# Kernel optimization log

Measured on AMD Instinct MI355X. Metric: run time of the kernel, lower is better.

Reference implementation:

```python
import jax, jax.numpy as jnp
import numpy as np

N = 100000   # nodes
E = 1600000  # edges (before self loops)
H = 2        # attention heads
C = 32       # per-head channels
EPS_BN = 1e-5
NEG_SLOPE = 0.2


def setup_inputs():
    key = jax.random.key(0)
    ks = jax.random.split(key, 32)
    s = 0.1
    inp = {
        "h": jax.random.normal(ks[0], (N, 2), jnp.float32),
        "edge_index": jax.random.randint(ks[1], (2, E), 0, N, dtype=jnp.int32),
        "bn_gamma": jnp.ones((2,), jnp.float32),
        "bn_beta": jnp.zeros((2,), jnp.float32),
        # GATConv 1: in=2 -> H*C=64
        "W1": jax.random.normal(ks[2], (H * C, 2), jnp.float32) * s,
        "as1": jax.random.normal(ks[3], (H, C), jnp.float32) * s,
        "ad1": jax.random.normal(ks[4], (H, C), jnp.float32) * s,
        "b1": jnp.zeros((H * C,), jnp.float32),
        # GATConv 2: in=64 -> 64
        "W2": jax.random.normal(ks[5], (H * C, 64), jnp.float32) * s,
        "as2": jax.random.normal(ks[6], (H, C), jnp.float32) * s,
        "ad2": jax.random.normal(ks[7], (H, C), jnp.float32) * s,
        "b2": jnp.zeros((H * C,), jnp.float32),
    }
    dims = [(64, 64), (64, 64), (64, 64), (64, 64), (11, 64)]
    for i, (o, ii) in enumerate(dims, start=1):
        inp[f"fw{i}"] = jax.random.normal(ks[8 + 2 * i], (o, ii), jnp.float32) * s
        inp[f"fb{i}"] = jnp.zeros((o,), jnp.float32)
    return inp


def _gat_layer(x, src, dst, W, a_src, a_dst, b):
    # x: [N, Fin] -> xp: [N, H, C]
    xp = (x @ W.T).reshape(N, H, C)
    e_src = jnp.einsum("nhc,hc->nh", xp, a_src)  # [N,H]
    e_dst = jnp.einsum("nhc,hc->nh", xp, a_dst)
    e = jax.nn.leaky_relu(e_src[src] + e_dst[dst], NEG_SLOPE)  # [Etot,H]
    # segment softmax over incoming edges of each dst node
    m = jax.ops.segment_max(e, dst, num_segments=N)            # [N,H]
    ex = jnp.exp(e - m[dst])
    denom = jax.ops.segment_sum(ex, dst, num_segments=N)
    alpha = ex / (denom[dst] + 1e-16)                          # [Etot,H]
    out = jax.ops.segment_sum(xp[src] * alpha[:, :, None], dst, num_segments=N)
    return out.reshape(N, H * C) + b


def reference(h, edge_index, bn_gamma, bn_beta,
              W1, as1, ad1, b1, W2, as2, ad2, b2,
              fw1, fb1, fw2, fb2, fw3, fb3, fw4, fb4, fw5, fb5):
    # BatchNorm1d (training mode: batch statistics, biased variance)
    mu = h.mean(0)
    var = ((h - mu) ** 2).mean(0)
    x = (h - mu) * jax.lax.rsqrt(var + EPS_BN) * bn_gamma + bn_beta

    # add self loops (PyG GATConv default)
    ar = jnp.arange(N, dtype=edge_index.dtype)
    src = jnp.concatenate([edge_index[0], ar])
    dst = jnp.concatenate([edge_index[1], ar])

    x = jax.nn.relu(_gat_layer(x, src, dst, W1, as1, ad1, b1))
    x = jax.nn.relu(_gat_layer(x, src, dst, W2, as2, ad2, b2))

    x = jax.nn.relu(x @ fw1.T + fb1)
    x = jax.nn.relu(x @ fw2.T + fb2)
    x = jax.nn.relu(x @ fw3.T + fb3)
    x = jax.nn.relu(x @ fw4.T + fb4)
    return x @ fw5.T + fb5
```

## Files before the change

### kernel.cpp

```cpp
#include <hip/hip_runtime.h>
#include <hip/hip_fp16.h>
#include <math.h>

#define NN 100000
#define EE 1600000
#define ET (EE + NN)
#define NEG 0.2f
#define SMASK 0x1FFFF

#define NBUCK 196
#define NBLK 416
#define BITEMS 4096
#define BCAP 10240

typedef float4 f4;
typedef _Float16 h8 __attribute__((ext_vector_type(8)));
typedef float f32x4 __attribute__((ext_vector_type(4)));

__global__ void k_init(float* stats, int* gcnt,
                       const float* __restrict__ W1, const float* __restrict__ as1,
                       const float* __restrict__ ad1, float* __restrict__ coef) {
    int i = threadIdx.x;
    if (i < 4) stats[i] = 0.f;
    if (i < NBUCK) gcnt[i] = 0;
    if (i >= 248) {
        int t = i - 248;
        int sd = t >> 2, hh = (t >> 1) & 1, c0 = t & 1;
        const float* a = sd ? ad1 : as1;
        float s = 0.f;
        for (int c = 0; c < 32; ++c) s += W1[(hh * 32 + c) * 2 + c0] * a[hh * 32 + c];
        coef[t] = s;
    }
}

__global__ void k_bnstats(const float* __restrict__ h, float* stats) {
    __shared__ float red[16];
    int gid = blockIdx.x * blockDim.x + threadIdx.x;
    int stride = gridDim.x * blockDim.x;
    float s0 = 0.f, s1 = 0.f, q0 = 0.f, q1 = 0.f;
    for (int i = gid; i < NN; i += stride) {
        float2 v = reinterpret_cast<const float2*>(h)[i];
        s0 += v.x; q0 += v.x * v.x;
        s1 += v.y; q1 += v.y * v.y;
    }
#pragma unroll
    for (int off = 32; off >= 1; off >>= 1) {
        s0 += __shfl_xor(s0, off);
        s1 += __shfl_xor(s1, off);
        q0 += __shfl_xor(q0, off);
        q1 += __shfl_xor(q1, off);
    }
    int wv = threadIdx.x >> 6;
    if ((threadIdx.x & 63) == 0) {
        red[wv * 4 + 0] = s0; red[wv * 4 + 1] = s1;
        red[wv * 4 + 2] = q0; red[wv * 4 + 3] = q1;
    }
    __syncthreads();
    if (threadIdx.x == 0) {
        float t0 = 0.f, t1 = 0.f, t2 = 0.f, t3 = 0.f;
#pragma unroll
        for (int i = 0; i < 4; ++i) {
            t0 += red[i * 4 + 0]; t1 += red[i * 4 + 1];
            t2 += red[i * 4 + 2]; t3 += red[i * 4 + 3];
        }
        atomicAdd(&stats[0], t0); atomicAdd(&stats[1], t1);
        atomicAdd(&stats[2], t2); atomicAdd(&stats[3], t3);
    }
}

__global__ void k_wprep(const float* __restrict__ W2g,
                        const float* __restrict__ w1, const float* __restrict__ w2,
                        const float* __restrict__ w3, const float* __restrict__ w4,
                        const float* __restrict__ w5,
                        _Float16* __restrict__ BH, _Float16* __restrict__ BL,
                        _Float16* __restrict__ BH5, _Float16* __restrict__ BL5) {
    int idx = blockIdx.x * blockDim.x + threadIdx.x;
    if (idx < 5 * 4096) {
        int L = idx >> 12;
        int r = idx & 4095;
        int ks = r >> 11, nt = (r >> 9) & 3, lane = (r >> 3) & 63, j = r & 7;
        const float* W = (L == 0) ? w1 : (L == 1) ? w2 : (L == 2) ? w3 : (L == 3) ? w4 : W2g;
        int n = nt * 16 + (lane & 15);
        int k = ks * 32 + 8 * (lane >> 4) + j;
        float v = W[n * 64 + k];
        _Float16 hi = (_Float16)v;
        BH[idx] = hi;
        BL[idx] = (_Float16)(v - (float)hi);
    }
    if (idx < 1024) {
        int ks = idx >> 9, lane = (idx >> 3) & 63, j = idx & 7;
        int n = lane & 15;
        int k = ks * 32 + 8 * (lane >> 4) + j;
        float v = (n < 11) ? w5[n * 64 + k] : 0.f;
        _Float16 hi = (_Float16)v;
        BH5[idx] = hi;
        BL5[idx] = (_Float16)(v - (float)hi);
    }
}

__global__ void __launch_bounds__(256) k_fpart(const int* __restrict__ ei, int* gcnt,
                                               unsigned* __restrict__ pairs) {
    __shared__ int hist[NBUCK];
    __shared__ int cur[NBUCK];
    int tid = threadIdx.x, blk = blockIdx.x;
    if (tid < NBUCK) hist[tid] = 0;
    int ss[16], dd[16];
    int base = blk * BITEMS;
    __syncthreads();
#pragma unroll
    for (int it = 0; it < 16; ++it) {
        int i = base + it * 256 + tid;
        int s = 0, d = -1;
        if (i < ET) {
            if (i < EE) { s = ei[i]; d = ei[EE + i]; }
            else { s = d = i - EE; }
            atomicAdd(&hist[d >> 9], 1);
        }
        ss[it] = s; dd[it] = d;
    }
    __syncthreads();
    if (tid < NBUCK) cur[tid] = tid * BCAP + atomicAdd(&gcnt[tid], hist[tid]);
    __syncthreads();
#pragma unroll
    for (int it = 0; it < 16; ++it) {
        int d = dd[it];
        if (d >= 0) {
            int pos = atomicAdd(&cur[d >> 9], 1);
            pairs[pos] = (unsigned)ss[it] | ((unsigned)(d & 511) << 17);
        }
    }
}

__global__ void __launch_bounds__(512) k_bucket(const unsigned* __restrict__ pairs,
                                                 const int* __restrict__ gcnt,
                                                 int* __restrict__ rowptr,
                                                 unsigned* __restrict__ srcl) {
    __shared__ int sh[512];
    __shared__ int se[512];
    int b = blockIdx.x, tid = threadIdx.x;
    sh[tid] = (tid < b) ? gcnt[tid] : 0;
    __syncthreads();
    for (int off = 256; off >= 1; off >>= 1) {
        if (tid < off) sh[tid] += sh[tid + off];
        __syncthreads();
    }
    int obase = sh[0];
    __syncthreads();
    int cnt = gcnt[b];
    int ibase = b * BCAP;
    sh[tid] = 0;
    __syncthreads();
    for (int k = tid; k < cnt; k += 512) atomicAdd(&sh[pairs[ibase + k] >> 17], 1);
    __syncthreads();
    int deg = sh[tid];
    se[tid] = deg;
    __syncthreads();
    for (int off = 1; off < 512; off <<= 1) {
        int t = (tid >= off) ? se[tid - off] : 0;
        __syncthreads();
        se[tid] += t;
        __syncthreads();
    }
    int excl = se[tid] - deg;
    int node = (b << 9) + tid;
    if (node < NN) rowptr[node] = obase + excl;
    sh[tid] = obase + excl;
    __syncthreads();
    for (int k = tid; k < cnt; k += 512) {
        unsigned p = pairs[ibase + k];
        int pos = atomicAdd(&sh[p >> 17], 1);
        srcl[pos] = p;
    }
    if (b == 0 && tid == 0) rowptr[NN] = ET;
}

__global__ void k_prep1(const float* __restrict__ h, const float* __restrict__ stats,
                        const float* __restrict__ gamma, const float* __restrict__ beta,
                        const float* __restrict__ coef,
                        f4* __restrict__ nd1, float2* __restrict__ ed1) {
    int n = blockIdx.x * blockDim.x + threadIdx.x;
    if (n >= NN) return;
    const float inv = 1.f / (float)NN;
    float mu0 = stats[0] * inv, mu1 = stats[1] * inv;
    float v0 = stats[2] * inv - mu0 * mu0;
    float v1 = stats[3] * inv - mu1 * mu1;
    float g0 = rsqrtf(v0 + 1e-5f) * gamma[0];
    float g1 = rsqrtf(v1 + 1e-5f) * gamma[1];
    float2 hv = reinterpret_cast<const float2*>(h)[n];
    float x0 = (hv.x - mu0) * g0 + beta[0];
    float x1 = (hv.y - mu1) * g1 + beta[1];
    nd1[n] = make_float4(x0 * coef[0] + x1 * coef[1], x0 * coef[2] + x1 * coef[3], x0, x1);
    ed1[n] = make_float2(x0 * coef[4] + x1 * coef[5], x0 * coef[6] + x1 * coef[7]);
}

__global__ void __launch_bounds__(256) k_gat1(
    const f4* __restrict__ nd1, const float2* __restrict__ ed1,
    const int* __restrict__ rowptr, const unsigned* __restrict__ srcl,
    f4* __restrict__ agg1a, float2* __restrict__ agg1s) {
    int gid = blockIdx.x * blockDim.x + threadIdx.x;
    int n = gid >> 3;
    int sub = gid & 7;
    if (n >= NN) return;
    int beg = rowptr[n], end = rowptr[n + 1];
    float2 ed = ed1[n];
    float A0 = 0.f, B0 = 0.f, S0 = 0.f, A1 = 0.f, B1 = 0.f, S1 = 0.f;
    for (int k = beg + sub; k < end; k += 8) {
        int s = (int)(srcl[k] & SMASK);
        f4 p = nd1[s];
        float e0 = p.x + ed.x;
        float e1 = p.y + ed.y;
        e0 = fmaxf(e0, NEG * e0);
        e1 = fmaxf(e1, NEG * e1);
        float w0 = __expf(e0);
        float w1 = __expf(e1);
        A0 += w0 * p.z; B0 += w0 * p.w; S0 += w0;
        A1 += w1 * p.z; B1 += w1 * p.w; S1 += w1;
    }
#pragma unroll
    for (int off = 1; off < 8; off <<= 1) {
        A0 += __shfl_xor(A0, off);
        B0 += __shfl_xor(B0, off);
        S0 += __shfl_xor(S0, off);
        A1 += __shfl_xor(A1, off);
        B1 += __shfl_xor(B1, off);
        S1 += __shfl_xor(S1, off);
    }
    if (sub == 0) {
        agg1a[n] = make_float4(A0, B0, A1, B1);
        agg1s[n] = make_float2(S0, S1);
    }
}

#define MAKE_A(ks)                                                                \
    f4 a0 = *reinterpret_cast<const f4*>(&xw[mrow * 68 + kg * 8 + (ks) * 32]);    \
    f4 a1 = *reinterpret_cast<const f4*>(&xw[mrow * 68 + kg * 8 + (ks) * 32 + 4]);\
    float av0 = a0.x, av1 = a0.y, av2 = a0.z, av3 = a0.w;                         \
    float av4 = a1.x, av5 = a1.y, av6 = a1.z, av7 = a1.w;                         \
    h8 ah, al;                                                                    \
    { _Float16 t;                                                                 \
      t = (_Float16)av0; ah[0] = t; al[0] = (_Float16)(av0 - (float)t);           \
      t = (_Float16)av1; ah[1] = t; al[1] = (_Float16)(av1 - (float)t);           \
      t = (_Float16)av2; ah[2] = t; al[2] = (_Float16)(av2 - (float)t);           \
      t = (_Float16)av3; ah[3] = t; al[3] = (_Float16)(av3 - (float)t);           \
      t = (_Float16)av4; ah[4] = t; al[4] = (_Float16)(av4 - (float)t);           \
      t = (_Float16)av5; ah[5] = t; al[5] = (_Float16)(av5 - (float)t);           \
      t = (_Float16)av6; ah[6] = t; al[6] = (_Float16)(av6 - (float)t);           \
      t = (_Float16)av7; ah[7] = t; al[7] = (_Float16)(av7 - (float)t); }

__global__ void __launch_bounds__(256) k_xform2m(
    const f4* __restrict__ agg1a, const float2* __restrict__ agg1s,
    const float* __restrict__ W1, const float* __restrict__ b1,
    const _Float16* __restrict__ BH2, const _Float16* __restrict__ BL2,
    const float* __restrict__ a_s, const float* __restrict__ a_d,
    __half* __restrict__ xph, float2* __restrict__ es2v, float2* __restrict__ ed2v) {
    __shared__ float xs[4 * 1088];
    int lane = threadIdx.x & 63;
    int w = threadIdx.x >> 6;
    float* xw = &xs[w * 1088];
    int nodeBase = blockIdx.x * 64 + w * 16;
    int mrow = lane & 15;
    int kg = lane >> 4;
    int n = nodeBase + mrow;

    f4 ag = make_float4(0.f, 0.f, 0.f, 0.f);
    float2 sg = make_float2(1.f, 1.f);
    if (n < NN) { ag = agg1a[n]; sg = agg1s[n]; }
    float r0 = 1.f / (sg.x + 1e-16f);
    float r1 = 1.f / (sg.y + 1e-16f);
#pragma unroll
    for (int j = 0; j < 16; ++j) {
        int f = kg * 16 + j;
        float A = (f < 32) ? ag.x : ag.z;
        float B = (f < 32) ? ag.y : ag.w;
        float r = (f < 32) ? r0 : r1;
        xw[mrow * 68 + f] = fmaxf((A * W1[2 * f] + B * W1[2 * f + 1]) * r + b1[f], 0.f);
    }
    __syncthreads();

    const h8* bh = reinterpret_cast<const h8*>(BH2);
    const h8* bl = reinterpret_cast<const h8*>(BL2);
    h8 BHr[2][4], BLr[2][4];
#pragma unroll
    for (int ks = 0; ks < 2; ++ks)
#pragma unroll
        for (int nt = 0; nt < 4; ++nt) {
            BHr[ks][nt] = bh[(ks * 4 + nt) * 64 + lane];
            BLr[ks][nt] = bl[(ks * 4 + nt) * 64 + lane];
        }
    f32x4 acc0 = {0.f, 0.f, 0.f, 0.f}, acc1 = acc0, acc2 = acc0, acc3 = acc0;
#pragma unroll
    for (int ks = 0; ks < 2; ++ks) {
        MAKE_A(ks)
        acc0 = __builtin_amdgcn_mfma_f32_16x16x32_f16(ah, BHr[ks][0], acc0, 0, 0, 0);
        acc1 = __builtin_amdgcn_mfma_f32_16x16x32_f16(ah, BHr[ks][1], acc1, 0, 0, 0);
        acc2 = __builtin_amdgcn_mfma_f32_16x16x32_f16(ah, BHr[ks][2], acc2, 0, 0, 0);
        acc3 = __builtin_amdgcn_mfma_f32_16x16x32_f16(ah, BHr[ks][3], acc3, 0, 0, 0);
        acc0 = __builtin_amdgcn_mfma_f32_16x16x32_f16(ah, BLr[ks][0], acc0, 0, 0, 0);
        acc1 = __builtin_amdgcn_mfma_f32_16x16x32_f16(ah, BLr[ks][1], acc1, 0, 0, 0);
        acc2 = __builtin_amdgcn_mfma_f32_16x16x32_f16(ah, BLr[ks][2], acc2, 0, 0, 0);
        acc3 = __builtin_amdgcn_mfma_f32_16x16x32_f16(ah, BLr[ks][3], acc3, 0, 0, 0);
        acc0 = __builtin_amdgcn_mfma_f32_16x16x32_f16(al, BHr[ks][0], acc0, 0, 0, 0);
        acc1 = __builtin_amdgcn_mfma_f32_16x16x32_f16(al, BHr[ks][1], acc1, 0, 0, 0);
        acc2 = __builtin_amdgcn_mfma_f32_16x16x32_f16(al, BHr[ks][2], acc2, 0, 0, 0);
        acc3 = __builtin_amdgcn_mfma_f32_16x16x32_f16(al, BHr[ks][3], acc3, 0, 0, 0);
    }
    __syncthreads();
#pragma unroll
    for (int r = 0; r < 4; ++r) {
        int row = 4 * kg + r;
        xw[row * 68 + mrow]      = acc0[r];
        xw[row * 68 + 16 + mrow] = acc1[r];
        xw[row * 68 + 32 + mrow] = acc2[r];
        xw[row * 68 + 48 + mrow] = acc3[r];
    }
    __syncthreads();

    float ps = 0.f, pd = 0.f;
#pragma unroll
    for (int j = 0; j < 16; ++j) {
        int f = kg * 16 + j;
        float v = xw[mrow * 68 + f];
        ps += v * a_s[f];
        pd += v * a_d[f];
    }
    ps += __shfl_xor(ps, 16);
    pd += __shfl_xor(pd, 16);
    float psB = __shfl_xor(ps, 32);
    float pdB = __shfl_xor(pd, 32);
    if (kg == 0 && n < NN) {
        es2v[n] = make_float2(ps, psB);
        ed2v[n] = make_float2(pd, pdB);
    }

#pragma unroll
    for (int i = 0; i < 8; ++i) {
        int idx = lane + 64 * i;
        int nl = idx >> 5;
        int c = idx & 31;
        int g = nodeBase + nl;
        if (g < NN) {
            __half2 hv = __floats2half2_rn(xw[nl * 68 + 2 * c], xw[nl * 68 + 2 * c + 1]);
            *reinterpret_cast<__half2*>(&xph[(size_t)g * 64 + 2 * c]) = hv;
        }
    }
}

__global__ void __launch_bounds__(256) k_gat2(
    const __half* __restrict__ xph, const float2* __restrict__ es2v,
    const float2* __restrict__ ed2v,
    const int* __restrict__ rowptr, const unsigned* __restrict__ srcl,
    const float* __restrict__ bias, float* __restrict__ y) {
    int wid = (blockIdx.x * blockDim.x + threadIdx.x) >> 6;
    int lane = threadIdx.x & 63;
    if (wid >= NN) return;
    int g = lane >> 3;
    int t = lane & 7;
    bool hh = t >= 4;
    int ch = 8 * t;
    float2 edp = ed2v[wid];
    float edv = hh ? edp.y : edp.x;
    int beg = rowptr[wid], end = rowptr[wid + 1];
    float sum = 0.f;
    float a0 = 0.f, a1 = 0.f, a2 = 0.f, a3 = 0.f;
    float a4 = 0.f, a5 = 0.f, a6 = 0.f, a7 = 0.f;
    int k = beg;

#define GO(kk)                                                                    \
    {                                                                             \
        int s_ = (int)(srcl[(kk) + g] & SMASK);                                   \
        float2 ep_ = es2v[s_];                                                    \
        uint4 xr_ = *reinterpret_cast<const uint4*>(&xph[(size_t)s_ * 64 + ch]);  \
        float e_ = (hh ? ep_.y : ep_.x) + edv;                                    \
        e_ = fmaxf(e_, NEG * e_);                                                 \
        float w_ = __expf(e_);                                                    \
        float2 p0_ = __half22float2(*reinterpret_cast<const __half2*>(&xr_.x));   \
        float2 p1_ = __half22float2(*reinterpret_cast<const __half2*>(&xr_.y));   \
        float2 p2_ = __half22float2(*reinterpret_cast<const __half2*>(&xr_.z));   \
        float2 p3_ = __half22float2(*reinterpret_cast<const __half2*>(&xr_.w));   \
        sum += w_;                                                                \
        a0 += w_ * p0_.x; a1 += w_ * p0_.y; a2 += w_ * p1_.x; a3 += w_ * p1_.y;   \
        a4 += w_ * p2_.x; a5 += w_ * p2_.y; a6 += w_ * p3_.x; a7 += w_ * p3_.y;   \
    }

    for (; k + 16 <= end; k += 16) {
        GO(k) GO(k + 8)
    }
    for (; k + 8 <= end; k += 8) {
        GO(k)
    }
    if (k < end) {
        int idx = k + g;
        bool valid = idx < end;
        int s_ = (int)(srcl[valid ? idx : k] & SMASK);
        float2 ep_ = es2v[s_];
        uint4 xr_ = *reinterpret_cast<const uint4*>(&xph[(size_t)s_ * 64 + ch]);
        float e_ = (hh ? ep_.y : ep_.x) + edv;
        e_ = fmaxf(e_, NEG * e_);
        float w_ = valid ? __expf(e_) : 0.f;
        float2 p0_ = __half22float2(*reinterpret_cast<const __half2*>(&xr_.x));
        float2 p1_ = __half22float2(*reinterpret_cast<const __half2*>(&xr_.y));
        float2 p2_ = __half22float2(*reinterpret_cast<const __half2*>(&xr_.z));
        float2 p3_ = __half22float2(*reinterpret_cast<const __half2*>(&xr_.w));
        sum += w_;
        a0 += w_ * p0_.x; a1 += w_ * p0_.y; a2 += w_ * p1_.x; a3 += w_ * p1_.y;
        a4 += w_ * p2_.x; a5 += w_ * p2_.y; a6 += w_ * p3_.x; a7 += w_ * p3_.y;
    }
#undef GO

#pragma unroll
    for (int off = 8; off <= 32; off <<= 1) {
        sum += __shfl_xor(sum, off);
        a0 += __shfl_xor(a0, off); a1 += __shfl_xor(a1, off);
        a2 += __shfl_xor(a2, off); a3 += __shfl_xor(a3, off);
        a4 += __shfl_xor(a4, off); a5 += __shfl_xor(a5, off);
        a6 += __shfl_xor(a6, off); a7 += __shfl_xor(a7, off);
    }
    if (lane < 8) {
        float rs = 1.f / (sum + 1e-16f);
        f4 r0v, r1v;
        r0v.x = fmaxf(a0 * rs + bias[ch], 0.f);
        r0v.y = fmaxf(a1 * rs + bias[ch + 1], 0.f);
        r0v.z = fmaxf(a2 * rs + bias[ch + 2], 0.f);
        r0v.w = fmaxf(a3 * rs + bias[ch + 3], 0.f);
        r1v.x = fmaxf(a4 * rs + bias[ch + 4], 0.f);
        r1v.y = fmaxf(a5 * rs + bias[ch + 5], 0.f);
        r1v.z = fmaxf(a6 * rs + bias[ch + 6], 0.f);
        r1v.w = fmaxf(a7 * rs + bias[ch + 7], 0.f);
        *reinterpret_cast<f4*>(&y[(size_t)wid * 64 + ch]) = r0v;
        *reinterpret_cast<f4*>(&y[(size_t)wid * 64 + ch + 4]) = r1v;
    }
}

__global__ void __launch_bounds__(256) k_mlp(
    const float* __restrict__ hin,
    const _Float16* __restrict__ BH, const _Float16* __restrict__ BL,
    const _Float16* __restrict__ BH5, const _Float16* __restrict__ BL5,
    const float* __restrict__ b1, const float* __restrict__ b2,
    const float* __restrict__ b3, const float* __restrict__ b4,
    const float* __restrict__ b5,
    float* __restrict__ out) {
    __shared__ float xs[4 * 16 * 68];
    int lane = threadIdx.x & 63;
    int w = threadIdx.x >> 6;
    float* xw = &xs[w * 1088];
    int nodeBase = blockIdx.x * 64 + w * 16;
    int mrow = lane & 15;
    int kg = lane >> 4;

#pragma unroll
    for (int i = 0; i < 4; ++i) {
        int v = lane + 64 * i;
        int nl = v >> 4;
        int c4 = v & 15;
        f4 t = make_float4(0.f, 0.f, 0.f, 0.f);
        if (nodeBase + nl < NN)
            t = reinterpret_cast<const f4*>(hin)[(size_t)(nodeBase + nl) * 16 + c4];
        *reinterpret_cast<f4*>(&xw[nl * 68 + c4 * 4]) = t;
    }
    __syncthreads();

#define MLP_LAYER(L, Bp)                                                          \
    {                                                                             \
        const h8* bh = reinterpret_cast<const h8*>(BH + (L) * 4096);              \
        const h8* bl = reinterpret_cast<const h8*>(BL + (L) * 4096);              \
        h8 BHr[2][4], BLr[2][4];                                                  \
        _Pragma("unroll")                                                         \
        for (int ks = 0; ks < 2; ++ks)                                            \
            _Pragma("unroll")                                                     \
            for (int nt = 0; nt < 4; ++nt) {                                      \
                BHr[ks][nt] = bh[(ks * 4 + nt) * 64 + lane];                      \
                BLr[ks][nt] = bl[(ks * 4 + nt) * 64 + lane];                      \
            }                                                                     \
        float bj0 = Bp[mrow], bj1 = Bp[16 + mrow];                                \
        float bj2 = Bp[32 + mrow], bj3 = Bp[48 + mrow];                           \
        f32x4 acc0 = {0.f, 0.f, 0.f, 0.f}, acc1 = acc0, acc2 = acc0, acc3 = acc0; \
        _Pragma("unroll")                                                         \
        for (int ks = 0; ks < 2; ++ks) {                                          \
            MAKE_A(ks)                                                            \
            acc0 = __builtin_amdgcn_mfma_f32_16x16x32_f16(ah, BHr[ks][0], acc0, 0, 0, 0); \
            acc1 = __builtin_amdgcn_mfma_f32_16x16x32_f16(ah, BHr[ks][1], acc1, 0, 0, 0); \
            acc2 = __builtin_amdgcn_mfma_f32_16x16x32_f16(ah, BHr[ks][2], acc2, 0, 0, 0); \
            acc3 = __builtin_amdgcn_mfma_f32_16x16x32_f16(ah, BHr[ks][3], acc3, 0, 0, 0); \
            acc0 = __builtin_amdgcn_mfma_f32_16x16x32_f16(ah, BLr[ks][0], acc0, 0, 0, 0); \
            acc1 = __builtin_amdgcn_mfma_f32_16x16x32_f16(ah, BLr[ks][1], acc1, 0, 0, 0); \
            acc2 = __builtin_amdgcn_mfma_f32_16x16x32_f16(ah, BLr[ks][2], acc2, 0, 0, 0); \
            acc3 = __builtin_amdgcn_mfma_f32_16x16x32_f16(ah, BLr[ks][3], acc3, 0, 0, 0); \
            acc0 = __builtin_amdgcn_mfma_f32_16x16x32_f16(al, BHr[ks][0], acc0, 0, 0, 0); \
            acc1 = __builtin_amdgcn_mfma_f32_16x16x32_f16(al, BHr[ks][1], acc1, 0, 0, 0); \
            acc2 = __builtin_amdgcn_mfma_f32_16x16x32_f16(al, BHr[ks][2], acc2, 0, 0, 0); \
            acc3 = __builtin_amdgcn_mfma_f32_16x16x32_f16(al, BHr[ks][3], acc3, 0, 0, 0); \
        }                                                                         \
        __syncthreads();                                                          \
        _Pragma("unroll")                                                         \
        for (int r = 0; r < 4; ++r) {                                             \
            int row = 4 * kg + r;                                                 \
            xw[row * 68 + mrow]      = fmaxf(acc0[r] + bj0, 0.f);                 \
            xw[row * 68 + 16 + mrow] = fmaxf(acc1[r] + bj1, 0.f);                 \
            xw[row * 68 + 32 + mrow] = fmaxf(acc2[r] + bj2, 0.f);                 \
            xw[row * 68 + 48 + mrow] = fmaxf(acc3[r] + bj3, 0.f);                 \
        }                                                                         \
        __syncthreads();                                                          \
    }

    MLP_LAYER(0, b1)
    MLP_LAYER(1, b2)
    MLP_LAYER(2, b3)
    MLP_LAYER(3, b4)
#undef MLP_LAYER

    {
        const h8* bh = reinterpret_cast<const h8*>(BH5);
        const h8* bl = reinterpret_cast<const h8*>(BL5);
        f32x4 acc = {0.f, 0.f, 0.f, 0.f};
#pragma unroll
        for (int ks = 0; ks < 2; ++ks) {
            MAKE_A(ks)
            h8 b_h = bh[ks * 64 + lane];
            h8 b_l = bl[ks * 64 + lane];
            acc = __builtin_amdgcn_mfma_f32_16x16x32_f16(ah, b_h, acc, 0, 0, 0);
            acc = __builtin_amdgcn_mfma_f32_16x16x32_f16(ah, b_l, acc, 0, 0, 0);
            acc = __builtin_amdgcn_mfma_f32_16x16x32_f16(al, b_h, acc, 0, 0, 0);
        }
        if (mrow < 11) {
            float b5v = b5[mrow];
#pragma unroll
            for (int r = 0; r < 4; ++r) {
                int node = nodeBase + 4 * kg + r;
                if (node < NN) out[(size_t)node * 11 + mrow] = acc[r] + b5v;
            }
        }
    }
}

extern "C" void kernel_launch(void* const* d_in, const int* in_sizes, int n_in,
                              void* d_out, int out_size, void* d_ws, size_t ws_size,
                              hipStream_t stream) {
    const float* h   = (const float*)d_in[0];
    const int*   ei  = (const int*)d_in[1];
    const float* gam = (const float*)d_in[2];
    const float* bet = (const float*)d_in[3];
    const float* W1  = (const float*)d_in[4];
    const float* as1 = (const float*)d_in[5];
    const float* ad1 = (const float*)d_in[6];
    const float* b1  = (const float*)d_in[7];
    const float* W2  = (const float*)d_in[8];
    const float* as2 = (const float*)d_in[9];
    const float* ad2 = (const float*)d_in[10];
    const float* b2  = (const float*)d_in[11];
    const float* fw1 = (const float*)d_in[12];
    const float* fb1 = (const float*)d_in[13];
    const float* fw2 = (const float*)d_in[14];
    const float* fb2 = (const float*)d_in[15];
    const float* fw3 = (const float*)d_in[16];
    const float* fb3 = (const float*)d_in[17];
    const float* fw4 = (const float*)d_in[18];
    const float* fb4 = (const float*)d_in[19];
    const float* fw5 = (const float*)d_in[20];
    const float* fb5 = (const float*)d_in[21];
    float* out = (float*)d_out;

    char* ws = (char*)d_ws;
    size_t off = 0;
    auto alloc = [&](size_t bytes) -> char* {
        char* p = ws + off;
        off += (bytes + 255) & ~(size_t)255;
        return p;
    };
    float* stats  = (float*)alloc(4 * sizeof(float));
    float* coef   = (float*)alloc(8 * sizeof(float));
    int*   gcnt   = (int*)alloc(NBUCK * sizeof(int));
    int*   rowptr = (int*)alloc((size_t)(NN + 1) * sizeof(int));
    unsigned* srcl = (unsigned*)alloc((size_t)ET * sizeof(unsigned));
    float2* es2v  = (float2*)alloc((size_t)NN * sizeof(float2));
    float2* ed2v  = (float2*)alloc((size_t)NN * sizeof(float2));
    _Float16* BH  = (_Float16*)alloc(5 * 4096 * sizeof(_Float16));
    _Float16* BL  = (_Float16*)alloc(5 * 4096 * sizeof(_Float16));
    _Float16* BH5 = (_Float16*)alloc(1024 * sizeof(_Float16));
    _Float16* BL5 = (_Float16*)alloc(1024 * sizeof(_Float16));
    float* bufA   = (float*)alloc((size_t)NN * 64 * sizeof(float));
    float* bufB   = (float*)alloc((size_t)NN * 64 * sizeof(float));
    unsigned* pairs = (unsigned*)bufA;
    __half* xph   = (__half*)bufA;
    f4*     agg1a = (f4*)bufB;
    float2* agg1s = (float2*)(bufB + 400000);
    f4*     nd1   = (f4*)(bufB + 600000);
    float2* ed1   = (float2*)(bufB + 1000000);
    (void)ws_size; (void)in_sizes; (void)n_in; (void)out_size;

    k_init<<<1, 256, 0, stream>>>(stats, gcnt, W1, as1, ad1, coef);
    k_bnstats<<<64, 256, 0, stream>>>(h, stats);
    k_wprep<<<96, 256, 0, stream>>>(W2, fw1, fw2, fw3, fw4, fw5, BH, BL, BH5, BL5);

    k_fpart<<<NBLK, 256, 0, stream>>>(ei, gcnt, pairs);
    k_bucket<<<NBUCK, 512, 0, stream>>>(pairs, gcnt, rowptr, srcl);

    k_prep1<<<(NN + 255) / 256, 256, 0, stream>>>(h, stats, gam, bet, coef, nd1, ed1);
    k_gat1<<<(NN * 8 + 255) / 256, 256, 0, stream>>>(nd1, ed1, rowptr, srcl, agg1a, agg1s);

    k_xform2m<<<(NN + 63) / 64, 256, 0, stream>>>(agg1a, agg1s, W1, b1,
                                                  BH + 4 * 4096, BL + 4 * 4096,
                                                  as2, ad2, xph, es2v, ed2v);

    k_gat2<<<(NN * 64) / 256, 256, 0, stream>>>(xph, es2v, ed2v, rowptr, srcl, b2, bufB);

    k_mlp<<<(NN + 63) / 64, 256, 0, stream>>>(bufB, BH, BL, BH5, BL5,
                                              fb1, fb2, fb3, fb4, fb5, out);
}
```

Baseline: 151.7 us.

## Merge setup kernels, fuse BN prep into bucket, store GAT2 output as fp16

Merges the init and weight-prep kernels into a single launch and folds the per-node BatchNorm/attention-coefficient prep into the bucket-sort kernel, cutting two kernel launches. It also makes the second GAT layer write its activations as fp16 and has the MLP read and widen them, halving that intermediate's traffic. The fp16 intermediate adds rounding error to the MLP input.

```diff
diff --git a/kernel.cpp b/kernel.cpp
--- a/kernel.cpp
+++ b/kernel.cpp
@@ -17,64 +17,29 @@
 typedef _Float16 h8 __attribute__((ext_vector_type(8)));
 typedef float f32x4 __attribute__((ext_vector_type(4)));
 
-__global__ void k_init(float* stats, int* gcnt,
-                       const float* __restrict__ W1, const float* __restrict__ as1,
-                       const float* __restrict__ ad1, float* __restrict__ coef) {
-    int i = threadIdx.x;
-    if (i < 4) stats[i] = 0.f;
-    if (i < NBUCK) gcnt[i] = 0;
-    if (i >= 248) {
-        int t = i - 248;
-        int sd = t >> 2, hh = (t >> 1) & 1, c0 = t & 1;
-        const float* a = sd ? ad1 : as1;
-        float s = 0.f;
-        for (int c = 0; c < 32; ++c) s += W1[(hh * 32 + c) * 2 + c0] * a[hh * 32 + c];
-        coef[t] = s;
-    }
-}
-
-__global__ void k_bnstats(const float* __restrict__ h, float* stats) {
-    __shared__ float red[16];
-    int gid = blockIdx.x * blockDim.x + threadIdx.x;
-    int stride = gridDim.x * blockDim.x;
-    float s0 = 0.f, s1 = 0.f, q0 = 0.f, q1 = 0.f;
-    for (int i = gid; i < NN; i += stride) {
-        float2 v = reinterpret_cast<const float2*>(h)[i];
-        s0 += v.x; q0 += v.x * v.x;
-        s1 += v.y; q1 += v.y * v.y;
-    }
-#pragma unroll
-    for (int off = 32; off >= 1; off >>= 1) {
-        s0 += __shfl_xor(s0, off);
-        s1 += __shfl_xor(s1, off);
-        q0 += __shfl_xor(q0, off);
-        q1 += __shfl_xor(q1, off);
-    }
-    int wv = threadIdx.x >> 6;
-    if ((threadIdx.x & 63) == 0) {
-        red[wv * 4 + 0] = s0; red[wv * 4 + 1] = s1;
-        red[wv * 4 + 2] = q0; red[wv * 4 + 3] = q1;
-    }
-    __syncthreads();
-    if (threadIdx.x == 0) {
-        float t0 = 0.f, t1 = 0.f, t2 = 0.f, t3 = 0.f;
-#pragma unroll
-        for (int i = 0; i < 4; ++i) {
-            t0 += red[i * 4 + 0]; t1 += red[i * 4 + 1];
-            t2 += red[i * 4 + 2]; t3 += red[i * 4 + 3];
-        }
-        atomicAdd(&stats[0], t0); atomicAdd(&stats[1], t1);
-        atomicAdd(&stats[2], t2); atomicAdd(&stats[3], t3);
-    }
-}
-
-__global__ void k_wprep(const float* __restrict__ W2g,
+__global__ void k_setup(float* stats, int* gcnt,
+                        const float* __restrict__ W1, const float* __restrict__ as1,
+                        const float* __restrict__ ad1, float* __restrict__ coef,
+                        const float* __restrict__ W2g,
                         const float* __restrict__ w1, const float* __restrict__ w2,
                         const float* __restrict__ w3, const float* __restrict__ w4,
                         const float* __restrict__ w5,
                         _Float16* __restrict__ BH, _Float16* __restrict__ BL,
                         _Float16* __restrict__ BH5, _Float16* __restrict__ BL5) {
     int idx = blockIdx.x * blockDim.x + threadIdx.x;
+    if (blockIdx.x == 0) {
+        int i = threadIdx.x;
+        if (i < 4) stats[i] = 0.f;
+        if (i < NBUCK) gcnt[i] = 0;
+        if (i >= 248) {
+            int t = i - 248;
+            int sd = t >> 2, hh = (t >> 1) & 1, c0 = t & 1;
+            const float* a = sd ? ad1 : as1;
+            float s = 0.f;
+            for (int c = 0; c < 32; ++c) s += W1[(hh * 32 + c) * 2 + c0] * a[hh * 32 + c];
+            coef[t] = s;
+        }
+    }
     if (idx < 5 * 4096) {
         int L = idx >> 12;
         int r = idx & 4095;
@@ -98,6 +63,41 @@
     }
 }
 
+__global__ void k_bnstats(const float* __restrict__ h, float* stats) {
+    __shared__ float red[16];
+    int gid = blockIdx.x * blockDim.x + threadIdx.x;
+    int stride = gridDim.x * blockDim.x;
+    float s0 = 0.f, s1 = 0.f, q0 = 0.f, q1 = 0.f;
+    for (int i = gid; i < NN; i += stride) {
+        float2 v = reinterpret_cast<const float2*>(h)[i];
+        s0 += v.x; q0 += v.x * v.x;
+        s1 += v.y; q1 += v.y * v.y;
+    }
+#pragma unroll
+    for (int off = 32; off >= 1; off >>= 1) {
+        s0 += __shfl_xor(s0, off);
+        s1 += __shfl_xor(s1, off);
+        q0 += __shfl_xor(q0, off);
+        q1 += __shfl_xor(q1, off);
+    }
+    int wv = threadIdx.x >> 6;
+    if ((threadIdx.x & 63) == 0) {
+        red[wv * 4 + 0] = s0; red[wv * 4 + 1] = s1;
+        red[wv * 4 + 2] = q0; red[wv * 4 + 3] = q1;
+    }
+    __syncthreads();
+    if (threadIdx.x == 0) {
+        float t0 = 0.f, t1 = 0.f, t2 = 0.f, t3 = 0.f;
+#pragma unroll
+        for (int i = 0; i < 4; ++i) {
+            t0 += red[i * 4 + 0]; t1 += red[i * 4 + 1];
+            t2 += red[i * 4 + 2]; t3 += red[i * 4 + 3];
+        }
+        atomicAdd(&stats[0], t0); atomicAdd(&stats[1], t1);
+        atomicAdd(&stats[2], t2); atomicAdd(&stats[3], t3);
+    }
+}
+
 __global__ void __launch_bounds__(256) k_fpart(const int* __restrict__ ei, int* gcnt,
                                                unsigned* __restrict__ pairs) {
     __shared__ int hist[NBUCK];
@@ -134,7 +134,13 @@
 __global__ void __launch_bounds__(512) k_bucket(const unsigned* __restrict__ pairs,
                                                  const int* __restrict__ gcnt,
                                                  int* __restrict__ rowptr,
-                                                 unsigned* __restrict__ srcl) {
+                                                 unsigned* __restrict__ srcl,
+                                                 const float* __restrict__ h,
+                                                 const float* __restrict__ stats,
+                                                 const float* __restrict__ gamma,
+                                                 const float* __restrict__ beta,
+                                                 const float* __restrict__ coef,
+                                                 f4* __restrict__ nd1, float2* __restrict__ ed1) {
     __shared__ int sh[512];
     __shared__ int se[512];
     int b = blockIdx.x, tid = threadIdx.x;
@@ -172,25 +178,20 @@
         srcl[pos] = p;
     }
     if (b == 0 && tid == 0) rowptr[NN] = ET;
-}
-
-__global__ void k_prep1(const float* __restrict__ h, const float* __restrict__ stats,
-                        const float* __restrict__ gamma, const float* __restrict__ beta,
-                        const float* __restrict__ coef,
-                        f4* __restrict__ nd1, float2* __restrict__ ed1) {
-    int n = blockIdx.x * blockDim.x + threadIdx.x;
-    if (n >= NN) return;
-    const float inv = 1.f / (float)NN;
-    float mu0 = stats[0] * inv, mu1 = stats[1] * inv;
-    float v0 = stats[2] * inv - mu0 * mu0;
-    float v1 = stats[3] * inv - mu1 * mu1;
-    float g0 = rsqrtf(v0 + 1e-5f) * gamma[0];
-    float g1 = rsqrtf(v1 + 1e-5f) * gamma[1];
-    float2 hv = reinterpret_cast<const float2*>(h)[n];
-    float x0 = (hv.x - mu0) * g0 + beta[0];
-    float x1 = (hv.y - mu1) * g1 + beta[1];
-    nd1[n] = make_float4(x0 * coef[0] + x1 * coef[1], x0 * coef[2] + x1 * coef[3], x0, x1);
-    ed1[n] = make_float2(x0 * coef[4] + x1 * coef[5], x0 * coef[6] + x1 * coef[7]);
+
+    if (node < NN) {
+        const float inv = 1.f / (float)NN;
+        float mu0 = stats[0] * inv, mu1 = stats[1] * inv;
+        float v0 = stats[2] * inv - mu0 * mu0;
+        float v1 = stats[3] * inv - mu1 * mu1;
+        float g0 = rsqrtf(v0 + 1e-5f) * gamma[0];
+        float g1 = rsqrtf(v1 + 1e-5f) * gamma[1];
+        float2 hv = reinterpret_cast<const float2*>(h)[node];
+        float x0 = (hv.x - mu0) * g0 + beta[0];
+        float x1 = (hv.y - mu1) * g1 + beta[1];
+        nd1[node] = make_float4(x0 * coef[0] + x1 * coef[1], x0 * coef[2] + x1 * coef[3], x0, x1);
+        ed1[node] = make_float2(x0 * coef[4] + x1 * coef[5], x0 * coef[6] + x1 * coef[7]);
+    }
 }
 
 __global__ void __launch_bounds__(256) k_gat1(
@@ -349,7 +350,7 @@
     const __half* __restrict__ xph, const float2* __restrict__ es2v,
     const float2* __restrict__ ed2v,
     const int* __restrict__ rowptr, const unsigned* __restrict__ srcl,
-    const float* __restrict__ bias, float* __restrict__ y) {
+    const float* __restrict__ bias, __half* __restrict__ yh) {
     int wid = (blockIdx.x * blockDim.x + threadIdx.x) >> 6;
     int lane = threadIdx.x & 63;
     if (wid >= NN) return;
@@ -417,22 +418,25 @@
     }
     if (lane < 8) {
         float rs = 1.f / (sum + 1e-16f);
-        f4 r0v, r1v;
-        r0v.x = fmaxf(a0 * rs + bias[ch], 0.f);
-        r0v.y = fmaxf(a1 * rs + bias[ch + 1], 0.f);
-        r0v.z = fmaxf(a2 * rs + bias[ch + 2], 0.f);
-        r0v.w = fmaxf(a3 * rs + bias[ch + 3], 0.f);
-        r1v.x = fmaxf(a4 * rs + bias[ch + 4], 0.f);
-        r1v.y = fmaxf(a5 * rs + bias[ch + 5], 0.f);
-        r1v.z = fmaxf(a6 * rs + bias[ch + 6], 0.f);
-        r1v.w = fmaxf(a7 * rs + bias[ch + 7], 0.f);
-        *reinterpret_cast<f4*>(&y[(size_t)wid * 64 + ch]) = r0v;
-        *reinterpret_cast<f4*>(&y[(size_t)wid * 64 + ch + 4]) = r1v;
+        __half2 o0 = __floats2half2_rn(fmaxf(a0 * rs + bias[ch], 0.f),
+                                       fmaxf(a1 * rs + bias[ch + 1], 0.f));
+        __half2 o1 = __floats2half2_rn(fmaxf(a2 * rs + bias[ch + 2], 0.f),
+                                       fmaxf(a3 * rs + bias[ch + 3], 0.f));
+        __half2 o2 = __floats2half2_rn(fmaxf(a4 * rs + bias[ch + 4], 0.f),
+                                       fmaxf(a5 * rs + bias[ch + 5], 0.f));
+        __half2 o3 = __floats2half2_rn(fmaxf(a6 * rs + bias[ch + 6], 0.f),
+                                       fmaxf(a7 * rs + bias[ch + 7], 0.f));
+        uint4 pk;
+        pk.x = *reinterpret_cast<unsigned*>(&o0);
+        pk.y = *reinterpret_cast<unsigned*>(&o1);
+        pk.z = *reinterpret_cast<unsigned*>(&o2);
+        pk.w = *reinterpret_cast<unsigned*>(&o3);
+        *reinterpret_cast<uint4*>(&yh[(size_t)wid * 64 + ch]) = pk;
     }
 }
 
 __global__ void __launch_bounds__(256) k_mlp(
-    const float* __restrict__ hin,
+    const __half* __restrict__ hin,
     const _Float16* __restrict__ BH, const _Float16* __restrict__ BL,
     const _Float16* __restrict__ BH5, const _Float16* __restrict__ BL5,
     const float* __restrict__ b1, const float* __restrict__ b2,
@@ -448,14 +452,21 @@
     int kg = lane >> 4;
 
 #pragma unroll
-    for (int i = 0; i < 4; ++i) {
-        int v = lane + 64 * i;
-        int nl = v >> 4;
-        int c4 = v & 15;
-        f4 t = make_float4(0.f, 0.f, 0.f, 0.f);
+    for (int i = 0; i < 2; ++i) {
+        int idx = lane + 64 * i;
+        int nl = idx >> 3;
+        int c8 = (idx & 7) * 8;
+        uint4 t = make_uint4(0u, 0u, 0u, 0u);
         if (nodeBase + nl < NN)
-            t = reinterpret_cast<const f4*>(hin)[(size_t)(nodeBase + nl) * 16 + c4];
-        *reinterpret_cast<f4*>(&xw[nl * 68 + c4 * 4]) = t;
+            t = *reinterpret_cast<const uint4*>(&hin[(size_t)(nodeBase + nl) * 64 + c8]);
+        float2 p0 = __half22float2(*reinterpret_cast<const __half2*>(&t.x));
+        float2 p1 = __half22float2(*reinterpret_cast<const __half2*>(&t.y));
+        float2 p2 = __half22float2(*reinterpret_cast<const __half2*>(&t.z));
+        float2 p3 = __half22float2(*reinterpret_cast<const __half2*>(&t.w));
+        f4 lo = make_float4(p0.x, p0.y, p1.x, p1.y);
+        f4 hi = make_float4(p2.x, p2.y, p3.x, p3.y);
+        *reinterpret_cast<f4*>(&xw[nl * 68 + c8]) = lo;
+        *reinterpret_cast<f4*>(&xw[nl * 68 + c8 + 4]) = hi;
     }
     __syncthreads();
 
@@ -585,24 +596,25 @@
     float2* agg1s = (float2*)(bufB + 400000);
     f4*     nd1   = (f4*)(bufB + 600000);
     float2* ed1   = (float2*)(bufB + 1000000);
+    __half* yh    = (__half*)bufB;
     (void)ws_size; (void)in_sizes; (void)n_in; (void)out_size;
 
-    k_init<<<1, 256, 0, stream>>>(stats, gcnt, W1, as1, ad1, coef);
+    k_setup<<<96, 256, 0, stream>>>(stats, gcnt, W1, as1, ad1, coef,
+                                    W2, fw1, fw2, fw3, fw4, fw5, BH, BL, BH5, BL5);
     k_bnstats<<<64, 256, 0, stream>>>(h, stats);
-    k_wprep<<<96, 256, 0, stream>>>(W2, fw1, fw2, fw3, fw4, fw5, BH, BL, BH5, BL5);
 
     k_fpart<<<NBLK, 256, 0, stream>>>(ei, gcnt, pairs);
-    k_bucket<<<NBUCK, 512, 0, stream>>>(pairs, gcnt, rowptr, srcl);
-
-    k_prep1<<<(NN + 255) / 256, 256, 0, stream>>>(h, stats, gam, bet, coef, nd1, ed1);
+    k_bucket<<<NBUCK, 512, 0, stream>>>(pairs, gcnt, rowptr, srcl,
+                                        h, stats, gam, bet, coef, nd1, ed1);
+
     k_gat1<<<(NN * 8 + 255) / 256, 256, 0, stream>>>(nd1, ed1, rowptr, srcl, agg1a, agg1s);
 
     k_xform2m<<<(NN + 63) / 64, 256, 0, stream>>>(agg1a, agg1s, W1, b1,
                                                   BH + 4 * 4096, BL + 4 * 4096,
                                                   as2, ad2, xph, es2v, ed2v);
 
-    k_gat2<<<(NN * 64) / 256, 256, 0, stream>>>(xph, es2v, ed2v, rowptr, srcl, b2, bufB);
-
-    k_mlp<<<(NN + 63) / 64, 256, 0, stream>>>(bufB, BH, BL, BH5, BL5,
+    k_gat2<<<(NN * 64) / 256, 256, 0, stream>>>(xph, es2v, ed2v, rowptr, srcl, b2, yh);
+
+    k_mlp<<<(NN + 63) / 64, 256, 0, stream>>>(yh, BH, BL, BH5, BL5,
                                               fb1, fb2, fb3, fb4, fb5, out);
 }
```

Result: faster. 145.9 us (-3.8%).
